# Kernel tuning notes

Measured on AMD Instinct MI355X. Metric: run time of the kernel, lower is better.

## Reference

```python
import jax, jax.numpy as jnp
import numpy as np
from jax import lax

BN_EPS = 1e-5


def conv3x3(x, w):
    # x: [B,C,H,W], w: [O,I,3,3] -> [B,O,H,W], stride 1, SAME padding, no bias
    return lax.conv_general_dilated(x, w, (1, 1), 'SAME',
                                    dimension_numbers=('NCHW', 'OIHW', 'NCHW'))


def batchnorm_eval(x, gamma, beta, mean, var):
    inv = gamma / jnp.sqrt(var + BN_EPS)
    return x * inv[None, :, None, None] + (beta - mean * inv)[None, :, None, None]


def avg_pool3(x):
    # AvgPool2d(3, stride=1, padding=1) with count_include_pad=True -> sum/9
    s = lax.reduce_window(x, 0.0, lax.add, (1, 1, 3, 3), (1, 1, 1, 1), 'SAME')
    return s / 9.0


def max_pool3(x):
    return lax.reduce_window(x, -jnp.inf, lax.max, (1, 1, 3, 3), (1, 1, 1, 1), 'SAME')


def setup_inputs() -> dict:
    key = jax.random.key(0)
    ks = jax.random.split(key, 20)
    B, C, H, W = 8, 256, 48, 48
    sc = 0.05
    inp = {
        'ftr': jax.random.normal(ks[0], (B, C, H, W), jnp.float32),
        'wq': jax.random.normal(ks[1], (C, C, 1, 1), jnp.float32) * sc,
        'bq': jax.random.normal(ks[2], (C,), jnp.float32) * sc,
        'wk': jax.random.normal(ks[3], (C, C, 1, 1), jnp.float32) * sc,
        'bk': jax.random.normal(ks[4], (C,), jnp.float32) * sc,
        'wv': jax.random.normal(ks[5], (C, C, 1, 1), jnp.float32) * sc,
        'bv': jax.random.normal(ks[6], (C,), jnp.float32) * sc,
        'delta': jnp.array([0.1], jnp.float32),
        'w_rbc': jax.random.normal(ks[7], (C, C, 3, 3), jnp.float32) * sc,
        'g1': jnp.ones((C,), jnp.float32),
        'b1': jnp.zeros((C,), jnp.float32),
        'm1': jnp.zeros((C,), jnp.float32),
        'v1': jnp.ones((C,), jnp.float32),
        'w_rbc2': jax.random.normal(ks[8], (C, 2 * C, 3, 3), jnp.float32) * sc,
        'g2': jnp.ones((C,), jnp.float32),
        'b2': jnp.zeros((C,), jnp.float32),
        'm2': jnp.zeros((C,), jnp.float32),
        'v2': jnp.ones((C,), jnp.float32),
    }
    return inp


def reference(ftr, wq, bq, wk, bk, wv, bv, delta, w_rbc, g1, b1, m1, v1,
              w_rbc2, g2, b2, m2, v2):
    B, C, H, W = ftr.shape
    P = H * W
    x = ftr.reshape(B, C, P)  # [B,C,P]
    # 1x1 convs as channel matmuls
    q = jnp.einsum('oc,bcp->bop', wq[:, :, 0, 0], x) + bq[None, :, None]
    k = jnp.einsum('oc,bcp->bop', wk[:, :, 0, 0], x) + bk[None, :, None]
    v = jnp.einsum('oc,bcp->bop', wv[:, :, 0, 0], x) + bv[None, :, None]
    # scores[b,i,j] = sum_c q[b,c,i] * k[b,c,j]; softmax over i (dim=1)
    scores = jnp.einsum('bci,bcj->bij', q, k)
    weights = jax.nn.softmax(scores, axis=1)
    G = jnp.einsum('bci,bij->bcj', v, weights).reshape(B, C, H, W)
    out = delta[0] * G + ftr
    # conv_rbc: conv3x3 -> BN(eval) -> ReLU, then sigmoid gate
    out = jax.nn.relu(batchnorm_eval(conv3x3(out, w_rbc), g1, b1, m1, v1))
    gate = jax.nn.sigmoid(out)
    ftr_avg = avg_pool3(ftr) * gate
    ftr_max = max_pool3(ftr) * gate
    cat = jnp.concatenate((ftr_max, ftr_avg), axis=1)  # [B,2C,H,W]
    out = jax.nn.relu(batchnorm_eval(conv3x3(cat, w_rbc2), g2, b2, m2, v2))
    return out
```

## Files before the change

### kernel.cpp

```cpp
#include <hip/hip_runtime.h>
#include <math.h>

#define NB   8
#define CCH  256
#define PPX  2304
#define CPb  (CCH*PPX)
#define NTOT (NB*CPb)
#define PSQ  (PPX*PPX)
#define PADIMG 2500

typedef short short8_t __attribute__((ext_vector_type(8)));
typedef float f4_t __attribute__((ext_vector_type(4)));

__device__ __forceinline__ float relu_(float x){ return x > 0.f ? x : 0.f; }

__device__ __forceinline__ unsigned short f2bf(float f) {
  unsigned int u = __builtin_bit_cast(unsigned int, f);
  u += 0x7fffu + ((u >> 16) & 1u);
  return (unsigned short)(u >> 16);
}
__device__ __forceinline__ float bf2f(unsigned short h) {
  unsigned int u = ((unsigned int)h) << 16;
  return __builtin_bit_cast(float, u);
}
__device__ __forceinline__ unsigned int pack2(float a, float b) {
  return (unsigned int)f2bf(a) | ((unsigned int)f2bf(b) << 16);
}

__device__ __forceinline__ void gll16(const void* g, void* l) {
  __builtin_amdgcn_global_load_lds(
      (const __attribute__((address_space(1))) unsigned int*)g,
      (__attribute__((address_space(3))) unsigned int*)l, 16, 0, 0);
}

__global__ __launch_bounds__(256) void castw(
    const float* __restrict__ w, unsigned short* __restrict__ o, int n)
{
  const int i = blockIdx.x * 256 + threadIdx.x;
  if (i < n) o[i] = f2bf(w[i]);
}

__global__ __launch_bounds__(256) void biascat(
    const float* __restrict__ a, const float* __restrict__ b,
    float* __restrict__ o)
{
  const int i = blockIdx.x * 256 + threadIdx.x;
  if (i < 256) o[i] = a[i];
  else if (i < 512) o[i] = b[i - 256];
}

__global__ __launch_bounds__(256) void border_clear(
    unsigned short* __restrict__ p, int C)
{
  const int idx = blockIdx.x * 256 + threadIdx.x;
  const int v4 = C >> 3;
  const int perB = 196 * v4;
  if (idx >= NB * perB) return;
  const int b = idx / perB;
  const int r = idx - b * perB;
  const int pos = r / v4;
  const int co = (r - pos * v4) * 8;
  int pp;
  if (pos < 50)        pp = pos;
  else if (pos < 100)  pp = 2450 + (pos - 50);
  else { const int j = pos - 100; pp = (1 + (j >> 1)) * 50 + (j & 1) * 49; }
  uint4 z; z.x = 0; z.y = 0; z.z = 0; z.w = 0;
  *(uint4*)(p + ((size_t)b * PADIMG + pp) * C + co) = z;
}

__global__ __launch_bounds__(256) void repack_w(
    const float* __restrict__ w, unsigned short* __restrict__ wr, int Cin)
{
  const int idx = blockIdx.x * 256 + threadIdx.x;
  const int total = 9 * 256 * Cin;
  if (idx >= total) return;
  const int c = idx % Cin;
  const int rest = idx / Cin;
  const int o = rest % 256;
  const int tap = rest / 256;
  wr[idx] = f2bf(w[((size_t)o * Cin + c) * 9 + tap]);
}

__global__ __launch_bounds__(256) void transpose_cast(
    const float* __restrict__ ftr, unsigned short* __restrict__ xt)
{
  const int p0 = blockIdx.x * 64, c0 = blockIdx.y * 64, b = blockIdx.z;
  const int t = threadIdx.x;
  __shared__ unsigned short T[64][72];
  #pragma unroll
  for (int pass = 0; pass < 4; pass++) {
    const int cr = pass * 16 + (t >> 4);
    const int pc = (t & 15) * 4;
    float4 v = *(const float4*)&ftr[((size_t)(b * 256 + c0 + cr)) * PPX + p0 + pc];
    T[pc + 0][cr] = f2bf(v.x); T[pc + 1][cr] = f2bf(v.y);
    T[pc + 2][cr] = f2bf(v.z); T[pc + 3][cr] = f2bf(v.w);
  }
  __syncthreads();
  #pragma unroll
  for (int pass = 0; pass < 2; pass++) {
    const int pr = pass * 32 + (t >> 3);
    const int cc = (t & 7) * 8;
    *(uint4*)&xt[((size_t)(b * PPX + p0 + pr)) * 256 + c0 + cc] = *(const uint4*)&T[pr][cc];
  }
}

template<int EPI>
__global__ __launch_bounds__(256) void gemm_nt(
    const unsigned short* __restrict__ A, long Ab,
    const unsigned short* __restrict__ B, long Bb, int K,
    unsigned short* __restrict__ O, long Ob, int ldo,
    const float* __restrict__ bias)
{
  const int t = threadIdx.x;
  const int ln = t & 63;
  const int wid = t >> 6;
  const int wm = (wid & 1) * 64, wn = (wid >> 1) * 64;
  const int lm = ln & 15, lg = ln >> 4;
  const int m0 = blockIdx.x * 128, n0 = blockIdx.y * 128;
  const long bz = blockIdx.z;
  const unsigned short* Ap = A + bz * Ab;
  const unsigned short* Bp = B + bz * Bb;

  __shared__ __align__(16) unsigned short As[128 * 32];
  __shared__ __align__(16) unsigned short Bs[128 * 32];

  const int sR = ln >> 2, sP = ln & 3;
  const int fbase = lm * 32 + (((lg + (lm >> 2)) & 3) * 8);

  f4_t acc[4][4];
  #pragma unroll
  for (int i = 0; i < 4; i++)
    #pragma unroll
    for (int j = 0; j < 4; j++) acc[i][j] = (f4_t){0.f, 0.f, 0.f, 0.f};

  for (int k0 = 0; k0 < K; k0 += 32) {
    __syncthreads();
    #pragma unroll
    for (int i = wid; i < 8; i += 4) {
      const int R = i * 16 + sR;
      const int l = (sP - (R >> 2)) & 3;
      gll16(Ap + (size_t)(m0 + R) * K + k0 + l * 8, As + i * 512);
      gll16(Bp + (size_t)(n0 + R) * K + k0 + l * 8, Bs + i * 512);
    }
    __syncthreads();
    short8_t a[4], b[4];
    #pragma unroll
    for (int ti = 0; ti < 4; ti++)
      a[ti] = *(const short8_t*)(As + (wm + ti * 16) * 32 + fbase);
    #pragma unroll
    for (int tj = 0; tj < 4; tj++)
      b[tj] = *(const short8_t*)(Bs + (wn + tj * 16) * 32 + fbase);
    #pragma unroll
    for (int ti = 0; ti < 4; ti++)
      #pragma unroll
      for (int tj = 0; tj < 4; tj++)
        acc[ti][tj] = __builtin_amdgcn_mfma_f32_16x16x32_bf16(
            a[ti], b[tj], acc[ti][tj], 0, 0, 0);
  }

  #pragma unroll
  for (int ti = 0; ti < 4; ti++) {
    const int mb = m0 + wm + ti * 16 + (lg << 2);
    #pragma unroll
    for (int tj = 0; tj < 4; tj++) {
      const int n = n0 + wn + tj * 16 + lm;
      float add0 = 0.f, add1 = 0.f, add2 = 0.f, add3 = 0.f;
      if (EPI == 2) { add0 = add1 = add2 = add3 = bias[n]; }
      uint2 o;
      o.x = pack2(acc[ti][tj][0] + add0, acc[ti][tj][1] + add1);
      o.y = pack2(acc[ti][tj][2] + add2, acc[ti][tj][3] + add3);
      *(uint2*)(O + bz * Ob + (size_t)n * ldo + mb) = o;
    }
  }
}

__global__ __launch_bounds__(256) void gemm_qk2(
    const unsigned short* __restrict__ A,
    const unsigned short* __restrict__ B, long Bb,
    unsigned short* __restrict__ Oq,
    const float* __restrict__ bias)
{
  const int t = threadIdx.x;
  const int ln = t & 63;
  const int wid = t >> 6;
  const int wm = (wid & 1) * 64, wn = (wid >> 1) * 64;
  const int lm = ln & 15, lg = ln >> 4;
  const int m0 = blockIdx.x * 128, n0 = blockIdx.y * 128;
  const long bz = blockIdx.z;
  const int K = 256;
  const unsigned short* Ap = A;
  const unsigned short* Bp = B + bz * Bb;

  __shared__ __align__(16) unsigned short As[128 * 32];
  __shared__ __align__(16) unsigned short Bs[128 * 32];

  const int sR = ln >> 2, sP = ln & 3;
  const int fbase = lm * 32 + (((lg + (lm >> 2)) & 3) * 8);

  f4_t acc[4][4];
  #pragma unroll
  for (int i = 0; i < 4; i++)
    #pragma unroll
    for (int j = 0; j < 4; j++) acc[i][j] = (f4_t){0.f, 0.f, 0.f, 0.f};

  for (int k0 = 0; k0 < K; k0 += 32) {
    __syncthreads();
    #pragma unroll
    for (int i = wid; i < 8; i += 4) {
      const int R = i * 16 + sR;
      const int l = (sP - (R >> 2)) & 3;
      gll16(Ap + (size_t)(m0 + R) * K + k0 + l * 8, As + i * 512);
      gll16(Bp + (size_t)(n0 + R) * K + k0 + l * 8, Bs + i * 512);
    }
    __syncthreads();
    short8_t a[4], b[4];
    #pragma unroll
    for (int ti = 0; ti < 4; ti++)
      a[ti] = *(const short8_t*)(As + (wm + ti * 16) * 32 + fbase);
    #pragma unroll
    for (int tj = 0; tj < 4; tj++)
      b[tj] = *(const short8_t*)(Bs + (wn + tj * 16) * 32 + fbase);
    #pragma unroll
    for (int ti = 0; ti < 4; ti++)
      #pragma unroll
      for (int tj = 0; tj < 4; tj++)
        acc[ti][tj] = __builtin_amdgcn_mfma_f32_16x16x32_bf16(
            a[ti], b[tj], acc[ti][tj], 0, 0, 0);
  }

  #pragma unroll
  for (int ti = 0; ti < 4; ti++) {
    const int mb = m0 + wm + ti * 16 + (lg << 2);
    const size_t obase = (mb >= 256 ? (size_t)NTOT : 0) + (size_t)bz * CPb;
    const int mc = mb & 255;
    #pragma unroll
    for (int tj = 0; tj < 4; tj++) {
      const int n = n0 + wn + tj * 16 + lm;
      uint2 o;
      o.x = pack2(acc[ti][tj][0] + bias[mb],     acc[ti][tj][1] + bias[mb + 1]);
      o.y = pack2(acc[ti][tj][2] + bias[mb + 2], acc[ti][tj][3] + bias[mb + 3]);
      *(uint2*)(Oq + obase + (size_t)n * 256 + mc) = o;
    }
  }
}

__global__ __launch_bounds__(256) void gemm_pv64(
    const unsigned short* __restrict__ A, long Ab,
    const unsigned short* __restrict__ B, long Bb,
    int K,
    unsigned short* __restrict__ O,
    const float* __restrict__ ftr, const float* __restrict__ delta, int bstart)
{
  const int t = threadIdx.x;
  const int ln = t & 63;
  const int wid = t >> 6;
  const int wm = (wid & 1) * 64, wn = (wid >> 1) * 32;
  const int lm = ln & 15, lg = ln >> 4;
  const int m0 = blockIdx.x * 128, n0 = blockIdx.y * 64;
  const long bz = blockIdx.z;
  const int b = bstart + (int)bz;
  const unsigned short* Ap = A + bz * Ab;
  const unsigned short* Bp = B + bz * Bb;

  __shared__ __align__(16) unsigned short As[128 * 32];
  __shared__ __align__(16) unsigned short Bs[64 * 32];

  const int sR = ln >> 2, sP = ln & 3;
  const int fbase = lm * 32 + (((lg + (lm >> 2)) & 3) * 8);

  f4_t acc[4][2];
  #pragma unroll
  for (int i = 0; i < 4; i++)
    #pragma unroll
    for (int j = 0; j < 2; j++) acc[i][j] = (f4_t){0.f, 0.f, 0.f, 0.f};

  for (int k0 = 0; k0 < K; k0 += 32) {
    __syncthreads();
    #pragma unroll
    for (int i = wid; i < 8; i += 4) {
      const int R = i * 16 + sR;
      const int l = (sP - (R >> 2)) & 3;
      gll16(Ap + (size_t)(m0 + R) * K + k0 + l * 8, As + i * 512);
    }
    {
      const int R = wid * 16 + sR;
      const int l = (sP - (R >> 2)) & 3;
      gll16(Bp + (size_t)(n0 + R) * K + k0 + l * 8, Bs + wid * 512);
    }
    __syncthreads();
    short8_t a[4], b8[2];
    #pragma unroll
    for (int ti = 0; ti < 4; ti++)
      a[ti] = *(const short8_t*)(As + (wm + ti * 16) * 32 + fbase);
    #pragma unroll
    for (int tj = 0; tj < 2; tj++)
      b8[tj] = *(const short8_t*)(Bs + (wn + tj * 16) * 32 + fbase);
    #pragma unroll
    for (int ti = 0; ti < 4; ti++)
      #pragma unroll
      for (int tj = 0; tj < 2; tj++)
        acc[ti][tj] = __builtin_amdgcn_mfma_f32_16x16x32_bf16(
            a[ti], b8[tj], acc[ti][tj], 0, 0, 0);
  }

  const float d0 = delta[0];
  #pragma unroll
  for (int ti = 0; ti < 4; ti++) {
    const int mb = m0 + wm + ti * 16 + (lg << 2);
    #pragma unroll
    for (int tj = 0; tj < 2; tj++) {
      const int n = n0 + wn + tj * 16 + lm;
      const int y = n / 48, x = n - (n / 48) * 48;
      const size_t pp = (size_t)(y + 1) * 50 + (x + 1);
      float vr[4];
      #pragma unroll
      for (int r = 0; r < 4; r++)
        vr[r] = d0 * acc[ti][tj][r] + ftr[((size_t)(b * 256 + mb + r)) * PPX + n];
      uint2 o;
      o.x = pack2(vr[0], vr[1]);
      o.y = pack2(vr[2], vr[3]);
      *(uint2*)(O + ((size_t)b * PADIMG + pp) * 256 + mb) = o;
    }
  }
}

__global__ __launch_bounds__(256) void rowstats(
    unsigned short* __restrict__ St, long sstride)
{
  const int j = blockIdx.x, bb = blockIdx.y;
  unsigned short* row = St + (long)bb * sstride + (size_t)j * PPX;
  const int t = threadIdx.x;

  float v[16];
  int nv = 0;
  float m = -1e30f;
  for (int ch = t; ch < 288; ch += 256) {
    const uint4 d = *(const uint4*)(row + ch * 8);
    const unsigned int* dp = (const unsigned int*)&d;
    #pragma unroll
    for (int q = 0; q < 4; q++) {
      v[nv]     = bf2f((unsigned short)(dp[q] & 0xffffu));
      v[nv + 1] = bf2f((unsigned short)(dp[q] >> 16));
      m = fmaxf(m, fmaxf(v[nv], v[nv + 1]));
      nv += 2;
    }
  }
  #pragma unroll
  for (int off = 32; off > 0; off >>= 1)
    m = fmaxf(m, __shfl_xor(m, off));
  __shared__ float red[8];
  if ((t & 63) == 0) red[t >> 6] = m;
  __syncthreads();
  m = fmaxf(fmaxf(red[0], red[1]), fmaxf(red[2], red[3]));

  float sum = 0.f;
  for (int u = 0; u < nv; u++) { v[u] = __expf(v[u] - m); sum += v[u]; }
  #pragma unroll
  for (int off = 32; off > 0; off >>= 1)
    sum += __shfl_xor(sum, off);
  if ((t & 63) == 0) red[4 + (t >> 6)] = sum;
  __syncthreads();
  const float inv = 1.f / (red[4] + red[5] + red[6] + red[7]);

  int u = 0;
  for (int ch = t; ch < 288; ch += 256) {
    unsigned int res[4];
    #pragma unroll
    for (int q = 0; q < 4; q++) {
      res[q] = pack2(v[u] * inv, v[u + 1] * inv);
      u += 2;
    }
    *(uint4*)(row + ch * 8) = *(const uint4*)res;
  }
}

template<bool OUT_BF16>
__global__ __launch_bounds__(256) void conv_mfma(
    const unsigned short* __restrict__ act_p, int Cin,
    const unsigned short* __restrict__ wr,
    const float* __restrict__ gamma, const float* __restrict__ beta,
    const float* __restrict__ mean,  const float* __restrict__ var,
    void* __restrict__ outv)
{
  const int t  = threadIdx.x;
  const int wv = t >> 6;
  const int ln = t & 63;
  const int lm = ln & 15;
  const int lg = ln >> 4;

  const int bx = blockIdx.x;
  const int bb = bx / 12;
  const int p0 = (bx % 12) * 192;
  const int m0 = blockIdx.y * 32;

  __shared__ __align__(16) unsigned short As[9 * 32 * 32];
  __shared__ __align__(16) unsigned short Bs[304 * 32];

  const int qbase = p0 + 2 * (p0 / 48);
  int qoff[3];
  #pragma unroll
  for (int tj = 0; tj < 3; tj++) {
    const int p = p0 + wv * 48 + tj * 16 + lm;
    qoff[tj] = (p - p0) + 2 * (p / 48 - p0 / 48) + 51;
  }

  const int sR = ln >> 2, sP = ln & 3;
  const int sl = (sP - (sR >> 2)) & 3;
  const int abase = lm * 32 + (((lg + (lm >> 2)) & 3) * 8);

  const unsigned short* gb = act_p + (size_t)bb * PADIMG * Cin + sl * 8;

  f4_t acc[2][3];
  #pragma unroll
  for (int i = 0; i < 2; i++)
    #pragma unroll
    for (int j = 0; j < 3; j++) acc[i][j] = (f4_t){0.f, 0.f, 0.f, 0.f};

  for (int c0 = 0; c0 < Cin; c0 += 32) {
    __syncthreads();
    for (int i = wv; i < 18; i += 4) {
      const int R = i * 16 + sR;
      const int tap = R >> 5, mr = R & 31;
      const int l = (sP - (R >> 2)) & 3;
      gll16(wr + ((size_t)(tap * 256 + m0 + mr)) * Cin + c0 + l * 8, As + i * 512);
    }
    for (int i = wv; i < 19; i += 4) {
      const int R = i * 16 + sR;
      int Rg = qbase + R;
      if (Rg > PADIMG - 1) Rg = PADIMG - 1;
      gll16(gb + (size_t)Rg * Cin + c0, Bs + i * 512);
    }
    __syncthreads();
    #pragma unroll
    for (int ky = 0; ky < 3; ky++) {
      #pragma unroll
      for (int kx = 0; kx < 3; kx++) {
        const int off = (ky - 1) * 50 + (kx - 1);
        const int tap = ky * 3 + kx;
        short8_t a[2], b[3];
        #pragma unroll
        for (int ti = 0; ti < 2; ti++)
          a[ti] = *(const short8_t*)(As + tap * 1024 + ti * 512 + abase);
        #pragma unroll
        for (int tj = 0; tj < 3; tj++) {
          const int R = qoff[tj] + off;
          const int slot = (lg + (R >> 2)) & 3;
          b[tj] = *(const short8_t*)(Bs + R * 32 + slot * 8);
        }
        #pragma unroll
        for (int ti = 0; ti < 2; ti++)
          #pragma unroll
          for (int tj = 0; tj < 3; tj++)
            acc[ti][tj] = __builtin_amdgcn_mfma_f32_16x16x32_bf16(
                a[ti], b[tj], acc[ti][tj], 0, 0, 0);
      }
    }
  }

  #pragma unroll
  for (int ti = 0; ti < 2; ti++) {
    const int m = m0 + ti * 16 + (lg << 2);
    float inv[4], add[4];
    #pragma unroll
    for (int r = 0; r < 4; r++) {
      inv[r] = gamma[m + r] * rsqrtf(var[m + r] + 1e-5f);
      add[r] = beta[m + r] - mean[m + r] * inv[r];
    }
    #pragma unroll
    for (int tj = 0; tj < 3; tj++) {
      const int p = p0 + wv * 48 + tj * 16 + lm;
      float vr[4];
      #pragma unroll
      for (int r = 0; r < 4; r++)
        vr[r] = relu_(acc[ti][tj][r] * inv[r] + add[r]);
      if (OUT_BF16) {
        uint2 o;
        o.x = pack2(vr[0], vr[1]);
        o.y = pack2(vr[2], vr[3]);
        *(uint2*)((unsigned short*)outv + ((size_t)(bb * PPX + p)) * 256 + m) = o;
      } else {
        #pragma unroll
        for (int r = 0; r < 4; r++)
          ((float*)outv)[((size_t)(bb * 256 + m + r)) * PPX + p] = vr[r];
      }
    }
  }
}

__global__ __launch_bounds__(256) void pool_gate_cat(
    const unsigned short* __restrict__ xt, const unsigned short* __restrict__ act1b,
    unsigned short* __restrict__ cat_p)
{
  const int idx = blockIdx.x * 256 + threadIdx.x;
  const int c = idx & 255;
  const int rest = idx >> 8;
  const int p = rest % PPX;
  const int b = rest / PPX;
  const int y = p / 48, x = p - (p / 48) * 48;
  const unsigned short* base = xt + ((size_t)b * PPX) * 256 + c;
  float s = 0.f, mxv = -1e30f;
  #pragma unroll
  for (int dy = -1; dy <= 1; dy++) {
    const int yy = y + dy;
    if (yy < 0 || yy >= 48) continue;
    #pragma unroll
    for (int dx = -1; dx <= 1; dx++) {
      const int xx = x + dx;
      if (xx < 0 || xx >= 48) continue;
      const float f = bf2f(base[(size_t)(yy * 48 + xx) * 256]);
      s += f; mxv = fmaxf(mxv, f);
    }
  }
  const float g = bf2f(act1b[(size_t)idx]);
  const float gate = 1.f / (1.f + __expf(-g));
  const size_t pp = (size_t)(y + 1) * 50 + (x + 1);
  unsigned short* crow = cat_p + ((size_t)b * PADIMG + pp) * 512;
  crow[c]       = f2bf(mxv * gate);
  crow[c + 256] = f2bf(s * (1.f / 9.f) * gate);
}

extern "C" void kernel_launch(void* const* d_in, const int* in_sizes, int n_in,
                              void* d_out, int out_size, void* d_ws, size_t ws_size,
                              hipStream_t stream)
{
  const float* ftr  = (const float*)d_in[0];
  const float* wq   = (const float*)d_in[1];
  const float* bq   = (const float*)d_in[2];
  const float* wk   = (const float*)d_in[3];
  const float* bk   = (const float*)d_in[4];
  const float* wv   = (const float*)d_in[5];
  const float* bv   = (const float*)d_in[6];
  const float* delta= (const float*)d_in[7];
  const float* w1   = (const float*)d_in[8];
  const float* g1   = (const float*)d_in[9];
  const float* b1   = (const float*)d_in[10];
  const float* m1   = (const float*)d_in[11];
  const float* v1   = (const float*)d_in[12];
  const float* w2   = (const float*)d_in[13];
  const float* g2   = (const float*)d_in[14];
  const float* b2   = (const float*)d_in[15];
  const float* m2   = (const float*)d_in[16];
  const float* v2   = (const float*)d_in[17];
  float* out = (float*)d_out;

  const size_t XT = (size_t)NTOT;
  unsigned short* base = (unsigned short*)d_ws;
  unsigned short* xt   = base;
  unsigned short* qt   = xt  + XT;
  unsigned short* kt   = qt  + XT;
  unsigned short* vbuf = kt  + XT;
  unsigned short* wqb  = vbuf + XT;
  unsigned short* wkb  = wqb + 65536;
  unsigned short* wvb  = wkb + 65536;
  unsigned short* wr1  = wvb + 65536;
  unsigned short* wr2  = wr1 + (size_t)9 * 256 * 256;
  unsigned short* attn_p = wr2 + (size_t)9 * 256 * 512;
  unsigned short* act1b  = attn_p + (size_t)NB * PADIMG * 256;
  unsigned short* cat_p  = act1b + XT;
  unsigned short* St     = cat_p + (size_t)NB * PADIMG * 512;

  float* bqk = (float*)act1b;

  const size_t head_bytes = (size_t)((char*)St - (char*)base);
  const bool modeA = ws_size >= head_bytes + (size_t)NB * PSQ * 2;

  castw<<<dim3(256), 256, 0, stream>>>(wq, wqb, 65536);
  castw<<<dim3(256), 256, 0, stream>>>(wk, wkb, 65536);
  castw<<<dim3(256), 256, 0, stream>>>(wv, wvb, 65536);
  biascat<<<dim3(2), 256, 0, stream>>>(bq, bk, bqk);
  repack_w<<<dim3((9 * 256 * 256 + 255) / 256), 256, 0, stream>>>(w1, wr1, 256);
  repack_w<<<dim3((9 * 256 * 512 + 255) / 256), 256, 0, stream>>>(w2, wr2, 512);

  transpose_cast<<<dim3(36, 4, 8), 256, 0, stream>>>(ftr, xt);

  gemm_qk2<<<dim3(4, 18, 8), 256, 0, stream>>>(wqb, xt, (long)CPb, qt, bqk);
  gemm_nt<2><<<dim3(18, 2, 8), 256, 0, stream>>>(
      xt, (long)CPb, wvb, 0L, 256, vbuf, (long)CPb, PPX, bv);

  border_clear<<<dim3(196), 256, 0, stream>>>(attn_p, 256);

  if (modeA) {
    gemm_nt<0><<<dim3(18, 18, 8), 256, 0, stream>>>(
        qt, (long)CPb, kt, (long)CPb, 256, St, (long)PSQ, PPX, nullptr);
    rowstats<<<dim3(PPX, 8), 256, 0, stream>>>(St, (long)PSQ);
    gemm_pv64<<<dim3(2, 36, 8), 256, 0, stream>>>(
        vbuf, (long)CPb, St, (long)PSQ, PPX, attn_p, ftr, delta, 0);
  } else {
    for (int b = 0; b < NB; b++) {
      gemm_nt<0><<<dim3(18, 18, 1), 256, 0, stream>>>(
          qt + (size_t)b * CPb, 0L, kt + (size_t)b * CPb, 0L, 256,
          St, 0L, PPX, nullptr);
      rowstats<<<dim3(PPX, 1), 256, 0, stream>>>(St, 0L);
      gemm_pv64<<<dim3(2, 36, 1), 256, 0, stream>>>(
          vbuf + (size_t)b * CPb, 0L, St, 0L, PPX, attn_p, ftr, delta, b);
    }
  }

  conv_mfma<true><<<dim3(96, 8), 256, 0, stream>>>(
      attn_p, 256, wr1, g1, b1, m1, v1, (void*)act1b);

  border_clear<<<dim3(392), 256, 0, stream>>>(cat_p, 512);
  pool_gate_cat<<<dim3(NTOT / 256), 256, 0, stream>>>(xt, act1b, cat_p);

  conv_mfma<false><<<dim3(96, 8), 256, 0, stream>>>(
      cat_p, 512, wr2, g2, b2, m2, v2, (void*)out);
}
```

Before: 416.8 us.

## Use larger 256x128 score GEMM tile, bf16 residual read, vectorized pool-gate kernel

```diff
diff --git a/kernel.cpp b/kernel.cpp
--- a/kernel.cpp
+++ b/kernel.cpp
@@ -174,6 +174,78 @@
   }
 }
 
+__global__ __launch_bounds__(256) void gemm_s(
+    const unsigned short* __restrict__ A, long Ab,
+    const unsigned short* __restrict__ B, long Bb,
+    unsigned short* __restrict__ O, long Ob, int ldo)
+{
+  const int K = 256;
+  const int t = threadIdx.x;
+  const int ln = t & 63;
+  const int wid = t >> 6;
+  const int wm = (wid & 1) * 128, wn = (wid >> 1) * 64;
+  const int lm = ln & 15, lg = ln >> 4;
+  const int m0 = blockIdx.x * 256, n0 = blockIdx.y * 128;
+  const long bz = blockIdx.z;
+  const unsigned short* Ap = A + bz * Ab;
+  const unsigned short* Bp = B + bz * Bb;
+
+  __shared__ __align__(16) unsigned short As[256 * 32];
+  __shared__ __align__(16) unsigned short Bs[128 * 32];
+
+  const int sR = ln >> 2, sP = ln & 3;
+  const int fbase = lm * 32 + (((lg + (lm >> 2)) & 3) * 8);
+
+  f4_t acc[8][4];
+  #pragma unroll
+  for (int i = 0; i < 8; i++)
+    #pragma unroll
+    for (int j = 0; j < 4; j++) acc[i][j] = (f4_t){0.f, 0.f, 0.f, 0.f};
+
+  for (int k0 = 0; k0 < K; k0 += 32) {
+    __syncthreads();
+    #pragma unroll
+    for (int i = wid; i < 16; i += 4) {
+      const int R = i * 16 + sR;
+      const int l = (sP - (R >> 2)) & 3;
+      gll16(Ap + (size_t)(m0 + R) * K + k0 + l * 8, As + i * 512);
+    }
+    #pragma unroll
+    for (int i = wid; i < 8; i += 4) {
+      const int R = i * 16 + sR;
+      const int l = (sP - (R >> 2)) & 3;
+      gll16(Bp + (size_t)(n0 + R) * K + k0 + l * 8, Bs + i * 512);
+    }
+    __syncthreads();
+    short8_t a[8], b[4];
+    #pragma unroll
+    for (int ti = 0; ti < 8; ti++)
+      a[ti] = *(const short8_t*)(As + (wm + ti * 16) * 32 + fbase);
+    #pragma unroll
+    for (int tj = 0; tj < 4; tj++)
+      b[tj] = *(const short8_t*)(Bs + (wn + tj * 16) * 32 + fbase);
+    #pragma unroll
+    for (int ti = 0; ti < 8; ti++)
+      #pragma unroll
+      for (int tj = 0; tj < 4; tj++)
+        acc[ti][tj] = __builtin_amdgcn_mfma_f32_16x16x32_bf16(
+            a[ti], b[tj], acc[ti][tj], 0, 0, 0);
+  }
+
+  #pragma unroll
+  for (int ti = 0; ti < 8; ti++) {
+    const int mb = m0 + wm + ti * 16 + (lg << 2);
+    #pragma unroll
+    for (int tj = 0; tj < 4; tj++) {
+      const int n = n0 + wn + tj * 16 + lm;
+      uint2 o;
+      o.x = pack2(acc[ti][tj][0], acc[ti][tj][1]);
+      o.y = pack2(acc[ti][tj][2], acc[ti][tj][3]);
+      *(uint2*)(O + bz * Ob + (size_t)n * ldo + mb) = o;
+    }
+  }
+}
+
 __global__ __launch_bounds__(256) void gemm_qk2(
     const unsigned short* __restrict__ A,
     const unsigned short* __restrict__ B, long Bb,
@@ -249,7 +321,8 @@
     const unsigned short* __restrict__ B, long Bb,
     int K,
     unsigned short* __restrict__ O,
-    const float* __restrict__ ftr, const float* __restrict__ delta, int bstart)
+    const unsigned short* __restrict__ X,
+    const float* __restrict__ delta, int bstart)
 {
   const int t = threadIdx.x;
   const int ln = t & 63;
@@ -312,10 +385,16 @@
       const int n = n0 + wn + tj * 16 + lm;
       const int y = n / 48, x = n - (n / 48) * 48;
       const size_t pp = (size_t)(y + 1) * 50 + (x + 1);
+      const uint2 xv = *(const uint2*)(X + ((size_t)b * PPX + n) * 256 + mb);
+      float fr[4];
+      fr[0] = bf2f((unsigned short)(xv.x & 0xffffu));
+      fr[1] = bf2f((unsigned short)(xv.x >> 16));
+      fr[2] = bf2f((unsigned short)(xv.y & 0xffffu));
+      fr[3] = bf2f((unsigned short)(xv.y >> 16));
       float vr[4];
       #pragma unroll
       for (int r = 0; r < 4; r++)
-        vr[r] = d0 * acc[ti][tj][r] + ftr[((size_t)(b * 256 + mb + r)) * PPX + n];
+        vr[r] = d0 * acc[ti][tj][r] + fr[r];
       uint2 o;
       o.x = pack2(vr[0], vr[1]);
       o.y = pack2(vr[2], vr[3]);
@@ -492,13 +571,15 @@
     unsigned short* __restrict__ cat_p)
 {
   const int idx = blockIdx.x * 256 + threadIdx.x;
-  const int c = idx & 255;
-  const int rest = idx >> 8;
+  const int cg = (idx & 31) * 8;
+  const int rest = idx >> 5;
   const int p = rest % PPX;
   const int b = rest / PPX;
-  const int y = p / 48, x = p - (p / 48) * 48;
-  const unsigned short* base = xt + ((size_t)b * PPX) * 256 + c;
-  float s = 0.f, mxv = -1e30f;
+  const int y = p / 48, x = p - y * 48;
+  const unsigned short* base = xt + ((size_t)b * PPX) * 256 + cg;
+  float s[8], mx[8];
+  #pragma unroll
+  for (int e = 0; e < 8; e++) { s[e] = 0.f; mx[e] = -1e30f; }
   #pragma unroll
   for (int dy = -1; dy <= 1; dy++) {
     const int yy = y + dy;
@@ -507,16 +588,34 @@
     for (int dx = -1; dx <= 1; dx++) {
       const int xx = x + dx;
       if (xx < 0 || xx >= 48) continue;
-      const float f = bf2f(base[(size_t)(yy * 48 + xx) * 256]);
-      s += f; mxv = fmaxf(mxv, f);
-    }
-  }
-  const float g = bf2f(act1b[(size_t)idx]);
-  const float gate = 1.f / (1.f + __expf(-g));
+      const uint4 d = *(const uint4*)&base[(size_t)(yy * 48 + xx) * 256];
+      const unsigned int* dp = (const unsigned int*)&d;
+      #pragma unroll
+      for (int q = 0; q < 4; q++) {
+        const float f0 = bf2f((unsigned short)(dp[q] & 0xffffu));
+        const float f1 = bf2f((unsigned short)(dp[q] >> 16));
+        s[2 * q] += f0; s[2 * q + 1] += f1;
+        mx[2 * q] = fmaxf(mx[2 * q], f0);
+        mx[2 * q + 1] = fmaxf(mx[2 * q + 1], f1);
+      }
+    }
+  }
+  const uint4 g4 = *(const uint4*)&act1b[((size_t)b * PPX + p) * 256 + cg];
+  const unsigned int* gp = (const unsigned int*)&g4;
+  unsigned int om[4], oa[4];
+  #pragma unroll
+  for (int q = 0; q < 4; q++) {
+    const float g0 = bf2f((unsigned short)(gp[q] & 0xffffu));
+    const float g1 = bf2f((unsigned short)(gp[q] >> 16));
+    const float gt0 = 1.f / (1.f + __expf(-g0));
+    const float gt1 = 1.f / (1.f + __expf(-g1));
+    om[q] = pack2(mx[2 * q] * gt0, mx[2 * q + 1] * gt1);
+    oa[q] = pack2(s[2 * q] * (1.f / 9.f) * gt0, s[2 * q + 1] * (1.f / 9.f) * gt1);
+  }
   const size_t pp = (size_t)(y + 1) * 50 + (x + 1);
-  unsigned short* crow = cat_p + ((size_t)b * PADIMG + pp) * 512;
-  crow[c]       = f2bf(mxv * gate);
-  crow[c + 256] = f2bf(s * (1.f / 9.f) * gate);
+  unsigned short* crow = cat_p + ((size_t)b * PADIMG + pp) * 512 + cg;
+  *(uint4*)crow = *(const uint4*)om;
+  *(uint4*)(crow + 256) = *(const uint4*)oa;
 }
 
 extern "C" void kernel_launch(void* const* d_in, const int* in_sizes, int n_in,
@@ -580,19 +679,18 @@
   border_clear<<<dim3(196), 256, 0, stream>>>(attn_p, 256);
 
   if (modeA) {
-    gemm_nt<0><<<dim3(18, 18, 8), 256, 0, stream>>>(
-        qt, (long)CPb, kt, (long)CPb, 256, St, (long)PSQ, PPX, nullptr);
+    gemm_s<<<dim3(9, 18, 8), 256, 0, stream>>>(
+        qt, (long)CPb, kt, (long)CPb, St, (long)PSQ, PPX);
     rowstats<<<dim3(PPX, 8), 256, 0, stream>>>(St, (long)PSQ);
     gemm_pv64<<<dim3(2, 36, 8), 256, 0, stream>>>(
-        vbuf, (long)CPb, St, (long)PSQ, PPX, attn_p, ftr, delta, 0);
+        vbuf, (long)CPb, St, (long)PSQ, PPX, attn_p, xt, delta, 0);
   } else {
     for (int b = 0; b < NB; b++) {
-      gemm_nt<0><<<dim3(18, 18, 1), 256, 0, stream>>>(
-          qt + (size_t)b * CPb, 0L, kt + (size_t)b * CPb, 0L, 256,
-          St, 0L, PPX, nullptr);
+      gemm_s<<<dim3(9, 18, 1), 256, 0, stream>>>(
+          qt + (size_t)b * CPb, 0L, kt + (size_t)b * CPb, 0L, St, 0L, PPX);
       rowstats<<<dim3(PPX, 1), 256, 0, stream>>>(St, 0L);
       gemm_pv64<<<dim3(2, 36, 1), 256, 0, stream>>>(
-          vbuf + (size_t)b * CPb, 0L, St, 0L, PPX, attn_p, ftr, delta, b);
+          vbuf + (size_t)b * CPb, 0L, St, 0L, PPX, attn_p, xt, delta, b);
     }
   }
 
@@ -600,7 +698,7 @@
       attn_p, 256, wr1, g1, b1, m1, v1, (void*)act1b);
 
   border_clear<<<dim3(392), 256, 0, stream>>>(cat_p, 512);
-  pool_gate_cat<<<dim3(NTOT / 256), 256, 0, stream>>>(xt, act1b, cat_p);
+  pool_gate_cat<<<dim3(NTOT / 8 / 256), 256, 0, stream>>>(xt, act1b, cat_p);
 
   conv_mfma<false><<<dim3(96, 8), 256, 0, stream>>>(
       cat_p, 512, wr2, g2, b2, m2, v2, (void*)out);
```

New measurement: 409.2 us. About the same (-1.8%).
